# Optimization experiments

Hardware: AMD Instinct MI355X
Metric: run time of the kernel (lower is better)

Reference implementation:

```python
import jax, jax.numpy as jnp
import numpy as np

K = 3          # kernel_size
PAD = 1        # (K-1)//2
KK = K * K


def setup_inputs() -> dict:
    key = jax.random.key(0)
    k0, k1, k2 = jax.random.split(key, 3)
    N, C, H, W, O = 4, 64, 128, 128, 64
    x = jax.random.normal(k0, (N, C, H, W), jnp.float32)
    # small offset-conv weights -> realistic sub-pixel-ish offsets
    w_off = jax.random.normal(k1, (2 * KK, C, K, K), jnp.float32) * 0.01
    b_off = jnp.zeros((2 * KK,), jnp.float32)
    w_def = jax.random.normal(k2, (O, C, K, K), jnp.float32) * (1.0 / np.sqrt(C * KK))
    b_def = jnp.zeros((O,), jnp.float32)
    return {"x": x, "w_off": w_off, "b_off": b_off, "w_def": w_def, "b_def": b_def}


def _conv2d_same(x, w, b):
    y = jax.lax.conv_general_dilated(
        x, w, window_strides=(1, 1), padding=[(PAD, PAD), (PAD, PAD)],
        dimension_numbers=("NCHW", "OIHW", "NCHW"))
    return y + b[None, :, None, None]


def reference(x, w_off, b_off, w_def, b_def):
    N, C, H, W = x.shape
    O = w_def.shape[0]

    # 1) offset-predicting conv: [N, 2*KK, H, W]
    off = _conv2d_same(x, w_off, b_off)
    off = off.reshape(N, KK, 2, H, W)
    dy, dx = off[:, :, 0], off[:, :, 1]            # [N, KK, H, W]

    # 2) sampling locations p = p0 + p_k + delta_p
    ki, kj = jnp.meshgrid(jnp.arange(K), jnp.arange(K), indexing="ij")
    ki = ki.reshape(KK).astype(x.dtype)
    kj = kj.reshape(KK).astype(x.dtype)
    py = jnp.arange(H, dtype=x.dtype)[None, None, :, None] + (ki - PAD)[None, :, None, None] + dy
    px = jnp.arange(W, dtype=x.dtype)[None, None, None, :] + (kj - PAD)[None, :, None, None] + dx

    # 3) bilinear sample with zero padding outside the feature map
    y0f = jnp.floor(py); x0f = jnp.floor(px)
    wy = py - y0f; wx = px - x0f                   # [N, KK, H, W]
    y0 = y0f.astype(jnp.int32); x0 = x0f.astype(jnp.int32)

    xflat = x.reshape(N, C, H * W)

    def gather(yi, xi):
        valid = ((yi >= 0) & (yi < H) & (xi >= 0) & (xi < W)).astype(x.dtype)
        idx = (jnp.clip(yi, 0, H - 1) * W + jnp.clip(xi, 0, W - 1)).reshape(N, 1, KK * H * W)
        v = jnp.take_along_axis(xflat, idx, axis=2).reshape(N, C, KK, H, W)
        return v * valid[:, None]                  # mask out-of-bounds -> 0

    v00 = gather(y0, x0)
    v01 = gather(y0, x0 + 1)
    v10 = gather(y0 + 1, x0)
    v11 = gather(y0 + 1, x0 + 1)

    wy_ = wy[:, None]; wx_ = wx[:, None]           # [N, 1, KK, H, W]
    sampled = (v00 * (1 - wy_) * (1 - wx_) + v01 * (1 - wy_) * wx_
               + v10 * wy_ * (1 - wx_) + v11 * wy_ * wx_)   # [N, C, KK, H, W]

    # 4) deformable conv accumulation: contract C and kernel taps
    out = jnp.einsum("nckhw,ock->nohw", sampled, w_def.reshape(O, C, KK))
    return out + b_def[None, :, None, None]
```

## Files before the change

### kernel.cpp

```cpp
#include <hip/hip_runtime.h>


#define HWSZ 16384
#define CIN  64
#define OUTC 64

typedef __attribute__((ext_vector_type(8))) short short8v;
typedef __attribute__((ext_vector_type(16))) float f32x16;

static __device__ __forceinline__ unsigned bf16rne(float f) {
    unsigned u = __float_as_uint(f);
    return (u + 0x7FFFu + ((u >> 16) & 1u)) >> 16;
}

__global__ __launch_bounds__(256) void prep_kernel(const float* __restrict__ w_off,
                                                   const float* __restrict__ w_def,
                                                   float* __restrict__ ws) {
    int i = blockIdx.x * 256 + threadIdx.x;
    if (i < 10368) {
        int cj = i / 18, ch = i % 18;
        ws[i] = w_off[ch * 576 + cj];
    }
    if (i < 73728) {
        unsigned short* wB = (unsigned short*)(ws + 16384);
        int j  = i & 7;
        int ln = (i >> 3) & 63;
        int hl = (i >> 9) & 1;
        int ot = (i >> 10) & 1;
        int s  = i >> 11;
        int kk = s >> 2, cq = s & 3;
        int hf = ln >> 5, r = ln & 31;
        int c  = cq * 16 + hf * 8 + j;
        int o  = ot * 32 + r;
        float wv = w_def[o * 576 + c * 9 + kk];
        unsigned hb = bf16rne(wv);
        if (hl == 0) {
            wB[i] = (unsigned short)hb;
        } else {
            float lo = wv - __uint_as_float(hb << 16);
            wB[i] = (unsigned short)bf16rne(lo);
        }
    }
}

__global__ __launch_bounds__(256) void xpose_kernel(const float* __restrict__ x,
                                                    float* __restrict__ xT) {
    __shared__ float lds[64 * 129];
    const int h = blockIdx.x;
    const int n = blockIdx.y;
    const int t = threadIdx.x;
    for (int i = t; i < 8192; i += 256) {
        int c = i >> 7, w = i & 127;
        lds[c * 129 + w] = x[((size_t)(n * 64 + c) * 128 + h) * 128 + w];
    }
    __syncthreads();
    for (int i = t; i < 8192; i += 256) {
        int w = i >> 6, c = i & 63;
        xT[((size_t)(n * 128 + h) * 128 + w) * 64 + c] = lds[c * 129 + w];
    }
}

__global__ __launch_bounds__(256) void offconv2_kernel(const float* __restrict__ xT,
                                                       const float* __restrict__ wofT,
                                                       const float* __restrict__ b_off,
                                                       float* __restrict__ off) {
    __shared__ float ldsA[64 * 19];
    __shared__ float ldsB[64 * 19];
    const int t = threadIdx.x;
    const int p = t & 63;
    const int cq = __builtin_amdgcn_readfirstlane(t >> 6);
    const int n = blockIdx.z;
    const int h = blockIdx.y * 4 + (p >> 4);
    const int w = blockIdx.x * 16 + (p & 15);

    float acc[18];
#pragma unroll
    for (int ch = 0; ch < 18; ++ch) acc[ch] = 0.f;

    const float* xb = xT + (size_t)n * (HWSZ * 64) + cq * 16;

#pragma unroll 1
    for (int jy = 0; jy < 3; ++jy) {
#pragma unroll 1
        for (int jx = 0; jx < 3; ++jx) {
            int hy = h + jy - 1, wx = w + jx - 1;
            bool v = (hy >= 0) && (hy < 128) && (wx >= 0) && (wx < 128);
            int hc = min(max(hy, 0), 127), wc = min(max(wx, 0), 127);
            float m = v ? 1.f : 0.f;
            const float* src = xb + (hc * 128 + wc) * 64;
            float4 v0 = *(const float4*)(src);
            float4 v1 = *(const float4*)(src + 4);
            float4 v2 = *(const float4*)(src + 8);
            float4 v3 = *(const float4*)(src + 12);
            float xv[16] = {v0.x, v0.y, v0.z, v0.w, v1.x, v1.y, v1.z, v1.w,
                            v2.x, v2.y, v2.z, v2.w, v3.x, v3.y, v3.z, v3.w};
            const float* wr0 = wofT + ((cq * 16) * 9 + (jy * 3 + jx)) * 18;
#pragma unroll
            for (int ci = 0; ci < 16; ++ci) {
                float s = xv[ci] * m;
                const float* wr = wr0 + ci * 162;
#pragma unroll
                for (int ch = 0; ch < 18; ++ch)
                    acc[ch] = fmaf(s, wr[ch], acc[ch]);
            }
        }
    }

    if (cq == 2) {
#pragma unroll
        for (int ch = 0; ch < 18; ++ch) ldsA[p * 19 + ch] = acc[ch];
    } else if (cq == 3) {
#pragma unroll
        for (int ch = 0; ch < 18; ++ch) ldsB[p * 19 + ch] = acc[ch];
    }
    __syncthreads();
    if (cq == 0) {
#pragma unroll
        for (int ch = 0; ch < 18; ++ch) acc[ch] += ldsA[p * 19 + ch];
    } else if (cq == 1) {
#pragma unroll
        for (int ch = 0; ch < 18; ++ch) acc[ch] += ldsB[p * 19 + ch];
    }
    __syncthreads();
    if (cq == 1) {
#pragma unroll
        for (int ch = 0; ch < 18; ++ch) ldsA[p * 19 + ch] = acc[ch];
    }
    __syncthreads();
    if (cq == 0) {
        float* op = off + ((size_t)(n * 128 + h) * 128 + w) * 20;
#pragma unroll
        for (int ch = 0; ch < 18; ++ch)
            op[ch] = acc[ch] + ldsA[p * 19 + ch] + b_off[ch];
    }
}

__global__ __launch_bounds__(256) void deform_mfma_kernel(
    const float* __restrict__ xT, const float* __restrict__ off20,
    const unsigned short* __restrict__ wB, const float* __restrict__ b_def,
    float* __restrict__ out) {
    __shared__ float lds[128 * 65];
    const int t = threadIdx.x;
    const int lane = t & 63;
    const int wv = t >> 6;
    const int r = lane & 31;
    const int hf = lane >> 5;
    const int h = blockIdx.x;
    const int n = blockIdx.y;
    const int w = wv * 32 + r;

    f32x16 acc0, acc1;
    const float bv0 = b_def[r], bv1 = b_def[32 + r];
#pragma unroll
    for (int i = 0; i < 16; ++i) { acc0[i] = bv0; acc1[i] = bv1; }

    const float* xb = xT + (size_t)n * (HWSZ * 64);
    const float* ob = off20 + ((size_t)(n * 128 + h) * 128 + w) * 20;
    const short8v* wb8 = (const short8v*)wB;

#pragma unroll 1
    for (int ky = 0; ky < 3; ++ky) {
#pragma unroll 1
        for (int kx = 0; kx < 3; ++kx) {
            const int kk = ky * 3 + kx;
            float2 d = *(const float2*)(ob + 2 * kk);
            float py  = (float)(h + ky - 1) + d.x;
            float pxx = (float)(w + kx - 1) + d.y;
            float y0f = floorf(py), x0f = floorf(pxx);
            float wy = py - y0f, wxf = pxx - x0f;
            int y0 = (int)y0f, x0 = (int)x0f;
            int y1 = y0 + 1, x1 = x0 + 1;
            bool vy0 = (y0 >= 0) && (y0 < 128), vy1 = (y1 >= 0) && (y1 < 128);
            bool vx0 = (x0 >= 0) && (x0 < 128), vx1 = (x1 >= 0) && (x1 < 128);
            int cy0 = min(max(y0, 0), 127), cy1 = min(max(y1, 0), 127);
            int cx0 = min(max(x0, 0), 127), cx1 = min(max(x1, 0), 127);
            float c00 = (vy0 && vx0) ? (1.f - wy) * (1.f - wxf) : 0.f;
            float c01 = (vy0 && vx1) ? (1.f - wy) * wxf : 0.f;
            float c10 = (vy1 && vx0) ? wy * (1.f - wxf) : 0.f;
            float c11 = (vy1 && vx1) ? wy * wxf : 0.f;
            const float* p00 = xb + (cy0 * 128 + cx0) * 64 + hf * 8;
            const float* p01 = xb + (cy0 * 128 + cx1) * 64 + hf * 8;
            const float* p10 = xb + (cy1 * 128 + cx0) * 64 + hf * 8;
            const float* p11 = xb + (cy1 * 128 + cx1) * 64 + hf * 8;

#pragma unroll
            for (int cq = 0; cq < 4; ++cq) {
                const int s = kk * 4 + cq;
                short8v Bh0 = wb8[(s * 4 + 0) * 64 + lane];
                short8v Bl0 = wb8[(s * 4 + 1) * 64 + lane];
                short8v Bh1 = wb8[(s * 4 + 2) * 64 + lane];
                short8v Bl1 = wb8[(s * 4 + 3) * 64 + lane];
                const int c0 = cq * 16;
                float4 a0 = *(const float4*)(p00 + c0);
                float4 a1 = *(const float4*)(p00 + c0 + 4);
                float4 b0 = *(const float4*)(p01 + c0);
                float4 b1 = *(const float4*)(p01 + c0 + 4);
                float4 g0 = *(const float4*)(p10 + c0);
                float4 g1 = *(const float4*)(p10 + c0 + 4);
                float4 e0 = *(const float4*)(p11 + c0);
                float4 e1 = *(const float4*)(p11 + c0 + 4);
                float smp[8];
                smp[0] = c00 * a0.x + c01 * b0.x + c10 * g0.x + c11 * e0.x;
                smp[1] = c00 * a0.y + c01 * b0.y + c10 * g0.y + c11 * e0.y;
                smp[2] = c00 * a0.z + c01 * b0.z + c10 * g0.z + c11 * e0.z;
                smp[3] = c00 * a0.w + c01 * b0.w + c10 * g0.w + c11 * e0.w;
                smp[4] = c00 * a1.x + c01 * b1.x + c10 * g1.x + c11 * e1.x;
                smp[5] = c00 * a1.y + c01 * b1.y + c10 * g1.y + c11 * e1.y;
                smp[6] = c00 * a1.z + c01 * b1.z + c10 * g1.z + c11 * e1.z;
                smp[7] = c00 * a1.w + c01 * b1.w + c10 * g1.w + c11 * e1.w;
                short8v Ah, Al;
#pragma unroll
                for (int j2 = 0; j2 < 8; ++j2) {
                    unsigned hb = bf16rne(smp[j2]);
                    Ah[j2] = (short)hb;
                    float lo = smp[j2] - __uint_as_float(hb << 16);
                    Al[j2] = (short)bf16rne(lo);
                }
                acc0 = __builtin_amdgcn_mfma_f32_32x32x16_bf16(Ah, Bh0, acc0, 0, 0, 0);
                acc0 = __builtin_amdgcn_mfma_f32_32x32x16_bf16(Al, Bh0, acc0, 0, 0, 0);
                acc0 = __builtin_amdgcn_mfma_f32_32x32x16_bf16(Ah, Bl0, acc0, 0, 0, 0);
                acc1 = __builtin_amdgcn_mfma_f32_32x32x16_bf16(Ah, Bh1, acc1, 0, 0, 0);
                acc1 = __builtin_amdgcn_mfma_f32_32x32x16_bf16(Al, Bh1, acc1, 0, 0, 0);
                acc1 = __builtin_amdgcn_mfma_f32_32x32x16_bf16(Ah, Bl1, acc1, 0, 0, 0);
            }
        }
    }

#pragma unroll
    for (int reg = 0; reg < 16; ++reg) {
        int rowpx = (reg & 3) + 8 * (reg >> 2) + 4 * hf;
        lds[(wv * 32 + rowpx) * 65 + r]      = acc0[reg];
        lds[(wv * 32 + rowpx) * 65 + 32 + r] = acc1[reg];
    }
    __syncthreads();
    float* op = out + ((size_t)(n * 64) * 128 + h) * 128;
#pragma unroll
    for (int it = 0; it < 32; ++it) {
        int idx = it * 256 + t;
        int o = idx >> 7, wc = idx & 127;
        op[(size_t)o * HWSZ + wc] = lds[wc * 65 + o];
    }
}

extern "C" void kernel_launch(void* const* d_in, const int* in_sizes, int n_in,
                              void* d_out, int out_size, void* d_ws, size_t ws_size,
                              hipStream_t stream) {
    const float* x     = (const float*)d_in[0];
    const float* w_off = (const float*)d_in[1];
    const float* b_off = (const float*)d_in[2];
    const float* w_def = (const float*)d_in[3];
    const float* b_def = (const float*)d_in[4];
    float* ws   = (float*)d_ws;
    float* outp = (float*)d_out;

    float* wofT  = ws;
    unsigned short* wB = (unsigned short*)(ws + 16384);
    float* xT    = ws + 53248;
    float* off20 = xT + 4194304;

    prep_kernel<<<288, 256, 0, stream>>>(w_off, w_def, ws);
    xpose_kernel<<<dim3(128, 4), 256, 0, stream>>>(x, xT);
    offconv2_kernel<<<dim3(8, 32, 4), 256, 0, stream>>>(xT, wofT, b_off, off20);
    deform_mfma_kernel<<<dim3(128, 4), 256, 0, stream>>>(xT, off20, wB, b_def, outp);
}
```

Measured before the change: 186.2 us.

## Split deform conv channels across waves and remap blocks for XCD locality

The deformable-conv kernel now gives each of the four waves a 16-channel slice of one 32-pixel tile. Partial accumulators are reduced across waves through LDS, so the grid grows from 512 to 2048 blocks and launch bounds request 4 blocks per CU. All three main kernels also use a flat 1D grid with a remap so that blocks landing on the same XCD handle neighbouring rows, which should improve L2 reuse of xT. The cost is extra LDS reduction traffic and barriers, and each wave now runs fewer MFMAs between sample loads.

```diff
diff --git a/kernel.cpp b/kernel.cpp
--- a/kernel.cpp
+++ b/kernel.cpp
@@ -46,8 +46,10 @@
 __global__ __launch_bounds__(256) void xpose_kernel(const float* __restrict__ x,
                                                     float* __restrict__ xT) {
     __shared__ float lds[64 * 129];
-    const int h = blockIdx.x;
-    const int n = blockIdx.y;
+    const int fid = blockIdx.x;
+    const int xcd = fid & 7, j = fid >> 3;
+    const int g = xcd * 64 + j;
+    const int n = g >> 7, h = g & 127;
     const int t = threadIdx.x;
     for (int i = t; i < 8192; i += 256) {
         int c = i >> 7, w = i & 127;
@@ -69,9 +71,13 @@
     const int t = threadIdx.x;
     const int p = t & 63;
     const int cq = __builtin_amdgcn_readfirstlane(t >> 6);
-    const int n = blockIdx.z;
-    const int h = blockIdx.y * 4 + (p >> 4);
-    const int w = blockIdx.x * 16 + (p & 15);
+    const int fid = blockIdx.x;
+    const int xcd = fid & 7, j = fid >> 3;
+    const int gr = xcd * 16 + (j >> 3);
+    const int xt = j & 7;
+    const int n = gr >> 5;
+    const int h = (gr & 31) * 4 + (p >> 4);
+    const int w = xt * 16 + (p & 15);
 
     float acc[18];
 #pragma unroll
@@ -135,28 +141,31 @@
     }
 }
 
-__global__ __launch_bounds__(256) void deform_mfma_kernel(
+__global__ __launch_bounds__(256, 4) void deform_mfma4_kernel(
     const float* __restrict__ xT, const float* __restrict__ off20,
     const unsigned short* __restrict__ wB, const float* __restrict__ b_def,
     float* __restrict__ out) {
-    __shared__ float lds[128 * 65];
+    __shared__ float lds[6208];
     const int t = threadIdx.x;
     const int lane = t & 63;
-    const int wv = t >> 6;
+    const int cq = __builtin_amdgcn_readfirstlane(t >> 6);
     const int r = lane & 31;
     const int hf = lane >> 5;
-    const int h = blockIdx.x;
-    const int n = blockIdx.y;
-    const int w = wv * 32 + r;
+    const int fid = blockIdx.x;
+    const int xcd = fid & 7, j = fid >> 3;
+    const int g = xcd * 64 + (j >> 2);
+    const int n = g >> 7, h = g & 127;
+    const int w0 = (j & 3) * 32;
+    const int w = w0 + r;
 
     f32x16 acc0, acc1;
-    const float bv0 = b_def[r], bv1 = b_def[32 + r];
-#pragma unroll
-    for (int i = 0; i < 16; ++i) { acc0[i] = bv0; acc1[i] = bv1; }
+#pragma unroll
+    for (int i = 0; i < 16; ++i) { acc0[i] = 0.f; acc1[i] = 0.f; }
 
     const float* xb = xT + (size_t)n * (HWSZ * 64);
     const float* ob = off20 + ((size_t)(n * 128 + h) * 128 + w) * 20;
     const short8v* wb8 = (const short8v*)wB;
+    const int c0 = cq * 16 + hf * 8;
 
 #pragma unroll 1
     for (int ky = 0; ky < 3; ++ky) {
@@ -178,67 +187,104 @@
             float c01 = (vy0 && vx1) ? (1.f - wy) * wxf : 0.f;
             float c10 = (vy1 && vx0) ? wy * (1.f - wxf) : 0.f;
             float c11 = (vy1 && vx1) ? wy * wxf : 0.f;
-            const float* p00 = xb + (cy0 * 128 + cx0) * 64 + hf * 8;
-            const float* p01 = xb + (cy0 * 128 + cx1) * 64 + hf * 8;
-            const float* p10 = xb + (cy1 * 128 + cx0) * 64 + hf * 8;
-            const float* p11 = xb + (cy1 * 128 + cx1) * 64 + hf * 8;
-
-#pragma unroll
-            for (int cq = 0; cq < 4; ++cq) {
-                const int s = kk * 4 + cq;
-                short8v Bh0 = wb8[(s * 4 + 0) * 64 + lane];
-                short8v Bl0 = wb8[(s * 4 + 1) * 64 + lane];
-                short8v Bh1 = wb8[(s * 4 + 2) * 64 + lane];
-                short8v Bl1 = wb8[(s * 4 + 3) * 64 + lane];
-                const int c0 = cq * 16;
-                float4 a0 = *(const float4*)(p00 + c0);
-                float4 a1 = *(const float4*)(p00 + c0 + 4);
-                float4 b0 = *(const float4*)(p01 + c0);
-                float4 b1 = *(const float4*)(p01 + c0 + 4);
-                float4 g0 = *(const float4*)(p10 + c0);
-                float4 g1 = *(const float4*)(p10 + c0 + 4);
-                float4 e0 = *(const float4*)(p11 + c0);
-                float4 e1 = *(const float4*)(p11 + c0 + 4);
-                float smp[8];
-                smp[0] = c00 * a0.x + c01 * b0.x + c10 * g0.x + c11 * e0.x;
-                smp[1] = c00 * a0.y + c01 * b0.y + c10 * g0.y + c11 * e0.y;
-                smp[2] = c00 * a0.z + c01 * b0.z + c10 * g0.z + c11 * e0.z;
-                smp[3] = c00 * a0.w + c01 * b0.w + c10 * g0.w + c11 * e0.w;
-                smp[4] = c00 * a1.x + c01 * b1.x + c10 * g1.x + c11 * e1.x;
-                smp[5] = c00 * a1.y + c01 * b1.y + c10 * g1.y + c11 * e1.y;
-                smp[6] = c00 * a1.z + c01 * b1.z + c10 * g1.z + c11 * e1.z;
-                smp[7] = c00 * a1.w + c01 * b1.w + c10 * g1.w + c11 * e1.w;
-                short8v Ah, Al;
-#pragma unroll
-                for (int j2 = 0; j2 < 8; ++j2) {
-                    unsigned hb = bf16rne(smp[j2]);
-                    Ah[j2] = (short)hb;
-                    float lo = smp[j2] - __uint_as_float(hb << 16);
-                    Al[j2] = (short)bf16rne(lo);
-                }
-                acc0 = __builtin_amdgcn_mfma_f32_32x32x16_bf16(Ah, Bh0, acc0, 0, 0, 0);
-                acc0 = __builtin_amdgcn_mfma_f32_32x32x16_bf16(Al, Bh0, acc0, 0, 0, 0);
-                acc0 = __builtin_amdgcn_mfma_f32_32x32x16_bf16(Ah, Bl0, acc0, 0, 0, 0);
-                acc1 = __builtin_amdgcn_mfma_f32_32x32x16_bf16(Ah, Bh1, acc1, 0, 0, 0);
-                acc1 = __builtin_amdgcn_mfma_f32_32x32x16_bf16(Al, Bh1, acc1, 0, 0, 0);
-                acc1 = __builtin_amdgcn_mfma_f32_32x32x16_bf16(Ah, Bl1, acc1, 0, 0, 0);
+
+            const int s = kk * 4 + cq;
+            short8v Bh0 = wb8[(s * 4 + 0) * 64 + lane];
+            short8v Bl0 = wb8[(s * 4 + 1) * 64 + lane];
+            short8v Bh1 = wb8[(s * 4 + 2) * 64 + lane];
+            short8v Bl1 = wb8[(s * 4 + 3) * 64 + lane];
+
+            const float* p00 = xb + (cy0 * 128 + cx0) * 64 + c0;
+            const float* p01 = xb + (cy0 * 128 + cx1) * 64 + c0;
+            const float* p10 = xb + (cy1 * 128 + cx0) * 64 + c0;
+            const float* p11 = xb + (cy1 * 128 + cx1) * 64 + c0;
+            float4 a0 = *(const float4*)(p00);
+            float4 a1 = *(const float4*)(p00 + 4);
+            float4 b0 = *(const float4*)(p01);
+            float4 b1 = *(const float4*)(p01 + 4);
+            float4 g0 = *(const float4*)(p10);
+            float4 g1 = *(const float4*)(p10 + 4);
+            float4 e0 = *(const float4*)(p11);
+            float4 e1 = *(const float4*)(p11 + 4);
+            float smp[8];
+            smp[0] = c00 * a0.x + c01 * b0.x + c10 * g0.x + c11 * e0.x;
+            smp[1] = c00 * a0.y + c01 * b0.y + c10 * g0.y + c11 * e0.y;
+            smp[2] = c00 * a0.z + c01 * b0.z + c10 * g0.z + c11 * e0.z;
+            smp[3] = c00 * a0.w + c01 * b0.w + c10 * g0.w + c11 * e0.w;
+            smp[4] = c00 * a1.x + c01 * b1.x + c10 * g1.x + c11 * e1.x;
+            smp[5] = c00 * a1.y + c01 * b1.y + c10 * g1.y + c11 * e1.y;
+            smp[6] = c00 * a1.z + c01 * b1.z + c10 * g1.z + c11 * e1.z;
+            smp[7] = c00 * a1.w + c01 * b1.w + c10 * g1.w + c11 * e1.w;
+            short8v Ah, Al;
+#pragma unroll
+            for (int j2 = 0; j2 < 8; ++j2) {
+                unsigned hb = bf16rne(smp[j2]);
+                Ah[j2] = (short)hb;
+                float lo = smp[j2] - __uint_as_float(hb << 16);
+                Al[j2] = (short)bf16rne(lo);
             }
-        }
-    }
-
-#pragma unroll
-    for (int reg = 0; reg < 16; ++reg) {
-        int rowpx = (reg & 3) + 8 * (reg >> 2) + 4 * hf;
-        lds[(wv * 32 + rowpx) * 65 + r]      = acc0[reg];
-        lds[(wv * 32 + rowpx) * 65 + 32 + r] = acc1[reg];
-    }
-    __syncthreads();
-    float* op = out + ((size_t)(n * 64) * 128 + h) * 128;
-#pragma unroll
-    for (int it = 0; it < 32; ++it) {
-        int idx = it * 256 + t;
-        int o = idx >> 7, wc = idx & 127;
-        op[(size_t)o * HWSZ + wc] = lds[wc * 65 + o];
+            acc0 = __builtin_amdgcn_mfma_f32_32x32x16_bf16(Ah, Bh0, acc0, 0, 0, 0);
+            acc0 = __builtin_amdgcn_mfma_f32_32x32x16_bf16(Al, Bh0, acc0, 0, 0, 0);
+            acc0 = __builtin_amdgcn_mfma_f32_32x32x16_bf16(Ah, Bl0, acc0, 0, 0, 0);
+            acc1 = __builtin_amdgcn_mfma_f32_32x32x16_bf16(Ah, Bh1, acc1, 0, 0, 0);
+            acc1 = __builtin_amdgcn_mfma_f32_32x32x16_bf16(Al, Bh1, acc1, 0, 0, 0);
+            acc1 = __builtin_amdgcn_mfma_f32_32x32x16_bf16(Ah, Bl1, acc1, 0, 0, 0);
+        }
+    }
+
+    if (cq == 2) {
+#pragma unroll
+        for (int reg = 0; reg < 16; ++reg) {
+            lds[reg * 64 + lane] = acc0[reg];
+            lds[1024 + reg * 64 + lane] = acc1[reg];
+        }
+    } else if (cq == 3) {
+#pragma unroll
+        for (int reg = 0; reg < 16; ++reg) {
+            lds[2048 + reg * 64 + lane] = acc0[reg];
+            lds[3072 + reg * 64 + lane] = acc1[reg];
+        }
+    }
+    __syncthreads();
+    if (cq == 0) {
+#pragma unroll
+        for (int reg = 0; reg < 16; ++reg) {
+            acc0[reg] += lds[reg * 64 + lane];
+            acc1[reg] += lds[1024 + reg * 64 + lane];
+        }
+    } else if (cq == 1) {
+#pragma unroll
+        for (int reg = 0; reg < 16; ++reg) {
+            acc0[reg] += lds[2048 + reg * 64 + lane];
+            acc1[reg] += lds[3072 + reg * 64 + lane];
+        }
+    }
+    __syncthreads();
+    if (cq == 1) {
+#pragma unroll
+        for (int reg = 0; reg < 16; ++reg) {
+            lds[reg * 64 + lane] = acc0[reg];
+            lds[1024 + reg * 64 + lane] = acc1[reg];
+        }
+    }
+    __syncthreads();
+    if (cq == 0) {
+#pragma unroll
+        for (int reg = 0; reg < 16; ++reg) {
+            float v0 = acc0[reg] + lds[reg * 64 + lane];
+            float v1 = acc1[reg] + lds[1024 + reg * 64 + lane];
+            int px = (reg & 3) + 8 * (reg >> 2) + 4 * hf;
+            lds[4096 + px * 66 + r]      = v0 + b_def[r];
+            lds[4096 + px * 66 + 32 + r] = v1 + b_def[32 + r];
+        }
+    }
+    __syncthreads();
+    float* op = out + (size_t)n * (OUTC * HWSZ) + h * 128 + w0;
+#pragma unroll
+    for (int i = 0; i < 8; ++i) {
+        int idx = i * 256 + t;
+        int o = idx >> 5, px = idx & 31;
+        op[(size_t)o * HWSZ + px] = lds[4096 + px * 66 + o];
     }
 }
 
@@ -259,7 +305,7 @@
     float* off20 = xT + 4194304;
 
     prep_kernel<<<288, 256, 0, stream>>>(w_off, w_def, ws);
-    xpose_kernel<<<dim3(128, 4), 256, 0, stream>>>(x, xT);
-    offconv2_kernel<<<dim3(8, 32, 4), 256, 0, stream>>>(xT, wofT, b_off, off20);
-    deform_mfma_kernel<<<dim3(128, 4), 256, 0, stream>>>(xT, off20, wB, b_def, outp);
-}
+    xpose_kernel<<<512, 256, 0, stream>>>(x, xT);
+    offconv2_kernel<<<1024, 256, 0, stream>>>(xT, wofT, b_off, off20);
+    deform_mfma4_kernel<<<2048, 256, 0, stream>>>(xT, off20, wB, b_def, outp);
+}
```

Measured after the change: 192.9 us. 1.04x slower.
